# Optimization experiments

Hardware: AMD Instinct MI355X
Metric: run time of the kernel (lower is better)

## Reference

```python
import jax, jax.numpy as jnp
import numpy as np

# Constants mirroring FFTGADBase(feature_extractor='none', Npre=2000, block_size=64, overlap=16)
L = 0.24            # diffusion step size l
K_COEF = 0.03       # K = exp(logk), logk = log(0.03) fixed in RGB mode
EPS = 1e-8
BLOCK_SIZE = 64
OVERLAP = 16
NPRE = 2000
FFT_STEPS = 10
VAR_THRESH = 0.1
UNIF_FRAC = 0.7
B, H, W = 2, 1024, 1024
SH, SW = 128, 128


def _g(x, K):
    # Perona-Malik edge-stopping function (repo's g)
    return 1.0 / (1.0 + (x * x) / (K * K))


def _c(feats, K):
    # diffusion coefficients from channel-mean absolute finite differences
    cv = _g(jnp.mean(jnp.abs(feats[:, :, 1:, :] - feats[:, :, :-1, :]), axis=1, keepdims=True), K)
    ch = _g(jnp.mean(jnp.abs(feats[:, :, :, 1:] - feats[:, :, :, :-1]), axis=1, keepdims=True), K)
    return cv, ch  # cv: [B,1,H-1,W], ch: [B,1,H,W-1]


def _diffuse_step(cv, ch, I, l=L):
    # anisotropic diffusion stencil update (transmissions between neighbors)
    dv = I[:, :, 1:, :] - I[:, :, :-1, :]
    dh = I[:, :, :, 1:] - I[:, :, :, :-1]
    tv = l * cv * dv
    th = l * ch * dh
    I = I - jnp.pad(tv, ((0, 0), (0, 0), (1, 0), (0, 0))) + jnp.pad(tv, ((0, 0), (0, 0), (0, 1), (0, 0)))
    I = I - jnp.pad(th, ((0, 0), (0, 0), (0, 0), (1, 0))) + jnp.pad(th, ((0, 0), (0, 0), (0, 0), (0, 1)))
    return I


def _adjust_step(img, source, mask_inv):
    b, c, h, w = img.shape
    sh, sw = source.shape[2], source.shape[3]
    fy, fx = h // sh, w // sw
    # AdaptiveAvgPool2d((sh,sw)) with exact divisor == uniform 8x8 mean pool
    img_ss = img.reshape(b, c, sh, fy, sw, fx).mean(axis=(3, 5))
    ratio_ss = source / (img_ss + EPS)
    ratio_ss = jnp.where(mask_inv, 1.0, ratio_ss)
    # F.interpolate(mode='nearest') with exact multiple == pixel repeat
    ratio = jnp.repeat(jnp.repeat(ratio_ss, fy, axis=2), fx, axis=3)
    return img * ratio


def _avgpool3(x):
    # F.avg_pool2d(x, 3, stride=1, padding=1), count_include_pad=True -> /9 everywhere
    s = jax.lax.reduce_window(x, 0.0, jax.lax.add, (1, 1, 3, 3), (1, 1, 1, 1),
                              [(0, 0), (0, 0), (1, 1), (1, 1)])
    return s / 9.0


def _uniform_regions(cv, ch):
    cv_var = _avgpool3(cv ** 2) - _avgpool3(cv) ** 2
    ch_var = _avgpool3(ch ** 2) - _avgpool3(ch) ** 2
    hm = min(cv_var.shape[2], ch_var.shape[2])
    wm = min(cv_var.shape[3], ch_var.shape[3])
    return (cv_var[:, :, :hm, :wm] < VAR_THRESH) & (ch_var[:, :, :hm, :wm] < VAR_THRESH)


def _fft_block(block, cv_b, ch_b):
    # Closed-form multi-step uniform-coefficient diffusion in the Fourier domain:
    # eigenvalue of one explicit diffusion step on periodic grid, raised to FFT_STEPS.
    cv_m = cv_b.mean(axis=(1, 2, 3), keepdims=True)  # [B,1,1,1]
    ch_m = ch_b.mean(axis=(1, 2, 3), keepdims=True)
    bh, bw = block.shape[-2], block.shape[-1]
    fy = jnp.arange(bh, dtype=jnp.float32)[:, None]
    fx = jnp.arange(bw // 2 + 1, dtype=jnp.float32)[None, :]
    lam = (1.0 - 2.0 * L * cv_m * (1.0 - jnp.cos(2.0 * jnp.pi * fy / bh))
               - 2.0 * L * ch_m * (1.0 - jnp.cos(2.0 * jnp.pi * fx / bw)))
    Fb = jnp.fft.rfft2(block)
    return jnp.fft.irfft2(Fb * (lam ** FFT_STEPS), s=(bh, bw)).astype(block.dtype)


def _fft_diffuse(depth, cv, ch, ur):
    b, c, h, w = depth.shape
    h_cv, w_cv = cv.shape[2], cv.shape[3]
    h_ch, w_ch = ch.shape[2], ch.shape[3]
    step = BLOCK_SIZE - OVERLAP
    for y in range(0, h, step):
        for x in range(0, w, step):
            ye, xe = min(y + BLOCK_SIZE, h), min(x + BLOCK_SIZE, w)
            cye, cxe = min(ye - 1, h_cv), min(xe, w_cv)
            hye, hxe = min(ye, h_ch), min(xe - 1, w_ch)
            if y >= cye or x >= cxe or y >= hye or x >= hxe:
                continue
            uye, uxe = min(ye, ur.shape[2]), min(xe, ur.shape[3])
            if y >= uye or x >= uxe:
                continue
            old = depth[:, :, y:ye, x:xe]
            new = _fft_block(old, cv[:, :, y:cye, x:cxe], ch[:, :, y:hye, x:hxe])
            unif = ur[:, :, y:uye, x:uxe].astype(jnp.float32).mean(axis=(1, 2, 3))
            apply_fft = (unif > UNIF_FRAC)[:, None, None, None]
            bh, bw = ye - y, xe - x
            by = jnp.ones((bh,), dtype=jnp.float32)
            if y > 0:
                n = min(OVERLAP, bh)
                by = by.at[:n].set(jnp.arange(n, dtype=jnp.float32) / OVERLAP)
            bx = jnp.ones((bw,), dtype=jnp.float32)
            if x > 0:
                n = min(OVERLAP, bw)
                bx = bx.at[:n].set(jnp.arange(n, dtype=jnp.float32) / OVERLAP)
            blend = by[:, None] * bx[None, :]
            merged = old * (1.0 - blend) + new * blend  # at (0,0) blend==1 -> direct write, as in torch
            merged = jnp.where(apply_fft, merged, old)
            depth = depth.at[:, :, y:ye, x:xe].set(merged)
    return depth


def _diffuse(img, guide, source, mask_inv):
    # RGB mode: guide_feats = cat([guide, img], 1); K = exp(logk) = 0.03
    feats = jnp.concatenate([guide, img], axis=1)
    cv, ch = _c(feats, K_COEF)
    ur = _uniform_regions(cv, ch)
    # Npre section runs under torch.no_grad()
    img0 = jax.lax.stop_gradient(img)
    cv0 = jax.lax.stop_gradient(cv)
    ch0 = jax.lax.stop_gradient(ch)
    img0 = _fft_diffuse(img0, cv0, ch0, ur)

    def body(I, _):
        I = _diffuse_step(cv0, ch0, I)
        I = _adjust_step(I, jax.lax.stop_gradient(source), mask_inv)
        return I, None

    y_pred, _ = jax.lax.scan(body, img0, None, length=min(500, NPRE))
    return y_pred, cv, ch


def setup_inputs() -> dict:
    key = jax.random.key(0)
    k1, k2, k3, k4 = jax.random.split(key, 4)
    guide = jax.random.normal(k1, (B, 3, H, W), dtype=jnp.float32)
    # keep depths safely > deps=0.1 so the shift branch is statically off
    source = jax.random.uniform(k2, (B, 1, SH, SW), dtype=jnp.float32) + 0.5
    mask_lr = jax.random.uniform(k3, (B, 1, SH, SW), dtype=jnp.float32)
    y_bicubic = jnp.repeat(jnp.repeat(source, H // SH, axis=2), W // SW, axis=3) \
                + 0.05 * jax.random.normal(k4, (B, 1, H, W), dtype=jnp.float32)
    return {"guide": guide, "source": source, "mask_lr": mask_lr, "y_bicubic": y_bicubic}


def reference(guide, source, mask_lr, y_bicubic):
    mask_inv = mask_lr < 0.5
    y_pred, cv, ch = _diffuse(y_bicubic, guide, source, mask_inv)
    return y_pred, cv, ch
```

## Files before the change

### kernel.cpp

```cpp
#include <hip/hip_runtime.h>

#define HH 1024
#define WW 1024
#define HW 1048576
#define NBLK 22

__device__ __forceinline__ float aload(const float* p)
{
    return __uint_as_float(__hip_atomic_load((const unsigned int*)p,
                           __ATOMIC_RELAXED, __HIP_MEMORY_SCOPE_AGENT));
}
__device__ __forceinline__ void astore(float* p, float v)
{
    __hip_atomic_store((unsigned int*)p, __float_as_uint(v),
                       __ATOMIC_RELAXED, __HIP_MEMORY_SCOPE_AGENT);
}

__global__ __launch_bounds__(256) void coeff_kernel(
    const float* __restrict__ guide, const float* __restrict__ img,
    float* __restrict__ cv, float* __restrict__ ch)
{
    int x = blockIdx.x * 256 + threadIdx.x;
    int y = blockIdx.y;
    int b = blockIdx.z;
    const float* g0 = guide + (size_t)b * 3 * HW;
    const float* im = img + (size_t)b * HW;
    int p = y * WW + x;
    float f0 = g0[p], f1 = g0[HW + p], f2 = g0[2 * HW + p], f3 = im[p];
    const float KK = 0.03f * 0.03f;
    if (y < HH - 1) {
        int q = p + WW;
        float s = fabsf(g0[q] - f0) + fabsf(g0[HW + q] - f1)
                + fabsf(g0[2 * HW + q] - f2) + fabsf(im[q] - f3);
        float t = s * 0.25f;
        cv[(size_t)b * 1023 * 1024 + p] = 1.0f / (1.0f + t * t / KK);
    }
    if (x < WW - 1) {
        int q = p + 1;
        float s = fabsf(g0[q] - f0) + fabsf(g0[HW + q] - f1)
                + fabsf(g0[2 * HW + q] - f2) + fabsf(im[q] - f3);
        float t = s * 0.25f;
        ch[(size_t)b * 1024 * 1023 + y * 1023 + x] = 1.0f / (1.0f + t * t / KK);
    }
}

__device__ __forceinline__ float block_reduce(float v, float* tmp)
{
    #pragma unroll
    for (int off = 32; off > 0; off >>= 1) v += __shfl_down(v, off);
    __syncthreads();
    if ((threadIdx.x & 63) == 0) tmp[threadIdx.x >> 6] = v;
    __syncthreads();
    return tmp[0] + tmp[1] + tmp[2] + tmp[3];
}

__global__ __launch_bounds__(256) void stats_kernel(
    const float* __restrict__ cv, const float* __restrict__ ch,
    float* __restrict__ cvmA, float* __restrict__ chmA, float* __restrict__ unifA)
{
    int iy = blockIdx.x, ix = blockIdx.y, b = blockIdx.z;
    int y0 = iy * 48, x0 = ix * 48;
    int ye = min(y0 + 64, HH), xe = min(x0 + 64, WW);
    int bh = ye - y0, bw = xe - x0;
    const float* cvb = cv + (size_t)b * 1023 * 1024;
    const float* chb = ch + (size_t)b * 1024 * 1023;
    int tid = threadIdx.x;

    int cnt_cv = (bh - 1) * bw;
    float s_cv = 0.f;
    for (int k = tid; k < cnt_cv; k += 256) {
        int r = k / bw, c = k - r * bw;
        s_cv += cvb[(y0 + r) * 1024 + x0 + c];
    }
    int cnt_ch = bh * (bw - 1);
    float s_ch = 0.f;
    for (int k = tid; k < cnt_ch; k += 256) {
        int r = k / (bw - 1), c = k - r * (bw - 1);
        s_ch += chb[(y0 + r) * 1023 + x0 + c];
    }
    int uh = min(ye, 1023) - y0, uw = min(xe, 1023) - x0;
    int cnt_u = uh * uw;
    float s_u = 0.f;
    for (int k = tid; k < cnt_u; k += 256) {
        int r = k / uw, c = k - r * uw;
        int py = y0 + r, px = x0 + c;
        float a1 = 0.f, a2 = 0.f;
        #pragma unroll
        for (int dy = -1; dy <= 1; ++dy)
            #pragma unroll
            for (int dx = -1; dx <= 1; ++dx) {
                int yy = py + dy, xx = px + dx;
                if (yy >= 0 && yy < 1023 && xx >= 0 && xx < 1024) {
                    float v = cvb[yy * 1024 + xx]; a1 += v; a2 += v * v;
                }
            }
        float va = a2 * (1.f / 9.f) - (a1 * (1.f / 9.f)) * (a1 * (1.f / 9.f));
        float b1 = 0.f, b2 = 0.f;
        #pragma unroll
        for (int dy = -1; dy <= 1; ++dy)
            #pragma unroll
            for (int dx = -1; dx <= 1; ++dx) {
                int yy = py + dy, xx = px + dx;
                if (yy >= 0 && yy < 1024 && xx >= 0 && xx < 1023) {
                    float v = chb[yy * 1023 + xx]; b1 += v; b2 += v * v;
                }
            }
        float vb = b2 * (1.f / 9.f) - (b1 * (1.f / 9.f)) * (b1 * (1.f / 9.f));
        s_u += (va < 0.1f && vb < 0.1f) ? 1.f : 0.f;
    }

    __shared__ float tmp[4];
    float t_cv = block_reduce(s_cv, tmp);
    float t_ch = block_reduce(s_ch, tmp);
    float t_u  = block_reduce(s_u, tmp);
    if (tid == 0) {
        int bi = (b * NBLK + iy) * NBLK + ix;
        cvmA[bi]  = t_cv / (float)cnt_cv;
        chmA[bi]  = t_ch / (float)cnt_ch;
        unifA[bi] = t_u / (float)cnt_u;
    }
}

__global__ __launch_bounds__(256) void fftblk_group(
    float* __restrict__ depth,
    const float* __restrict__ cvmA, const float* __restrict__ chmA,
    const float* __restrict__ unifA, unsigned int* __restrict__ ftags,
    int base)
{
    int rem = base + (int)blockIdx.x;
    int iy = 0, ix = 0;
    for (int d = 0; d < 64; ++d) {
        int lo = (d > 21) ? ((d - 20) >> 1) : 0;
        int hi = ((d >> 1) < 21) ? (d >> 1) : 21;
        int wd = hi - lo + 1;
        if (rem < wd) { iy = lo + rem; ix = d - 2 * iy; break; }
        rem -= wd;
    }
    int b = blockIdx.y;
    int bi = (b * NBLK + iy) * NBLK + ix;
    int tid = threadIdx.x;

    bool active = (unifA[bi] > 0.7f);
    int y0 = iy * 48, x0 = ix * 48;
    int bh = min(64, HH - y0), bw = min(64, WW - x0);
    const int RH = bh >> 4;
    const int RW = bw >> 4;
    const int ty = tid >> 4, tx = tid & 15;
    float* gbase = depth + (size_t)b * HW + y0 * WW + x0;

    float cur[4][4], orig[4][4];
    if (active) {
        #pragma unroll
        for (int r = 0; r < 4; ++r)
            #pragma unroll
            for (int c = 0; c < 4; ++c)
                if (r < RH && c < RW) {
                    int i = RH * ty + r, j = RW * tx + c;
                    if (i >= 16 && j >= 16) {
                        float v = aload(gbase + i * WW + j);
                        cur[r][c] = v; orig[r][c] = v;
                    }
                }
    }

    {
        bool act = false; int di = 0, dj = 0;
        if (tid == 0) { act = (ix > 0);            di = iy;     dj = ix - 1; }
        if (tid == 1) { act = (iy > 0 && ix > 0);  di = iy - 1; dj = ix - 1; }
        if (tid == 2) { act = (iy > 0);            di = iy - 1; dj = ix;     }
        if (tid == 3) { act = (iy > 0 && ix < 21); di = iy - 1; dj = ix + 1; }
        if (tid < 4 && act) {
            const unsigned int* tp = ftags + (((b * NBLK + di) * NBLK + dj) << 4);
            int guard = 0;
            while (__hip_atomic_load(tp, __ATOMIC_RELAXED,
                                     __HIP_MEMORY_SCOPE_AGENT) < 1u) {
                if (++guard > (1 << 22)) break;
            }
        }
    }
    __syncthreads();

    if (active) {
        float av = 0.24f * cvmA[bi];
        float ah = 0.24f * chmA[bi];

        #pragma unroll
        for (int r = 0; r < 4; ++r)
            #pragma unroll
            for (int c = 0; c < 4; ++c)
                if (r < RH && c < RW) {
                    int i = RH * ty + r, j = RW * tx + c;
                    if (i < 16 || j < 16) {
                        float v = aload(gbase + i * WW + j);
                        cur[r][c] = v; orig[r][c] = v;
                    }
                }

        __shared__ float rT[2][16][65];
        __shared__ float rB[2][16][65];
        __shared__ float cL[2][16][65];
        __shared__ float cR[2][16][65];

        for (int it = 0; it < 10; ++it) {
            const int p = it & 1;
            #pragma unroll
            for (int c = 0; c < 4; ++c)
                if (c < RW) {
                    rT[p][ty][RW * tx + c] = cur[0][c];
                    rB[p][ty][RW * tx + c] = (RH == 4) ? cur[3][c] : cur[0][c];
                }
            #pragma unroll
            for (int r = 0; r < 4; ++r)
                if (r < RH) {
                    cL[p][tx][RH * ty + r] = cur[r][0];
                    cR[p][tx][RH * ty + r] = (RW == 4) ? cur[r][3] : cur[r][0];
                }
            __syncthreads();

            float nxt[4][4];
            #pragma unroll
            for (int r = 0; r < 4; ++r)
                #pragma unroll
                for (int c = 0; c < 4; ++c)
                    if (r < RH && c < RW) {
                        float ce = cur[r][c];
                        float up = (r > 0) ? cur[r - 1][c]
                                           : rB[p][(ty - 1) & 15][RW * tx + c];
                        float dn = rT[p][(ty + 1) & 15][RW * tx + c];
                        if (r + 1 < 4) { if (r + 1 < RH) dn = cur[r + 1][c]; }
                        float lf = (c > 0) ? cur[r][c - 1]
                                           : cR[p][(tx - 1) & 15][RH * ty + r];
                        float rt = cL[p][(tx + 1) & 15][RH * ty + r];
                        if (c + 1 < 4) { if (c + 1 < RW) rt = cur[r][c + 1]; }
                        nxt[r][c] = ce + av * (up + dn - 2.f * ce)
                                       + ah * (lf + rt - 2.f * ce);
                    }
            #pragma unroll
            for (int r = 0; r < 4; ++r)
                #pragma unroll
                for (int c = 0; c < 4; ++c)
                    if (r < RH && c < RW) cur[r][c] = nxt[r][c];
        }

        const float inv16 = 1.f / 16.f;
        #pragma unroll
        for (int r = 0; r < 4; ++r)
            #pragma unroll
            for (int c = 0; c < 4; ++c)
                if (r < RH && c < RW) {
                    int i = RH * ty + r, j = RW * tx + c;
                    float wy = (y0 > 0 && i < 16) ? (float)i * inv16 : 1.f;
                    float wx = (x0 > 0 && j < 16) ? (float)j * inv16 : 1.f;
                    float w = wy * wx;
                    astore(gbase + i * WW + j,
                           orig[r][c] * (1.f - w) + cur[r][c] * w);
                }
        asm volatile("s_waitcnt vmcnt(0)" ::: "memory");
    }
    __syncthreads();
    if (tid == 0)
        __hip_atomic_store(ftags + (bi << 4), 1u, __ATOMIC_RELAXED,
                           __HIP_MEMORY_SCOPE_AGENT);
}

__global__ __launch_bounds__(256, 4) void iter_kernel(
    const float* __restrict__ Iin, float* __restrict__ Iout,
    const float* __restrict__ cv, const float* __restrict__ ch,
    const float* __restrict__ source, const float* __restrict__ mask)
{
    const int w = blockIdx.x;
    const int xcd = w & 7, j = w >> 3;
    const int grb = xcd * 32 + (j >> 2);
    const int b  = grb >> 7;
    const int r0 = (grb & 127) * 8;
    const int c0 = (j & 3) * 256;
    const int tid = threadIdx.x;
    __shared__ float sI[10][258];
    const float* Ib  = Iin + (size_t)b * HW;
    const float* cvb = cv + (size_t)b * 1023 * 1024;
    const float* chb = ch + (size_t)b * 1024 * 1023;

    for (int k = tid; k < 10 * 258; k += 256) {
        int r = k / 258, c = k - r * 258;
        int gy = r0 - 1 + r, gx = c0 - 1 + c;
        float v = 0.f;
        if (gy >= 0 && gy < HH && gx >= 0 && gx < WW) v = Ib[gy * WW + gx];
        sI[r][c] = v;
    }

    const int gx = c0 + tid;
    float cvv[9];
    #pragma unroll
    for (int k = 0; k < 9; ++k) {
        int gr = r0 - 1 + k;
        cvv[k] = (gr >= 0 && gr < 1023) ? cvb[gr * 1024 + gx] : 0.f;
    }
    float chl[8], chh[8];
    #pragma unroll
    for (int k = 0; k < 8; ++k) {
        int rr = r0 + k;
        chh[k] = (gx < 1023) ? chb[rr * 1023 + gx] : 0.f;
        chl[k] = (gx > 0)    ? chb[rr * 1023 + gx - 1] : 0.f;
    }
    __syncthreads();

    float o[8];
    #pragma unroll
    for (int r = 0; r < 8; ++r) {
        float c  = sI[r + 1][tid + 1];
        float up = sI[r][tid + 1], dn = sI[r + 2][tid + 1];
        float lf = sI[r + 1][tid], rt = sI[r + 1][tid + 2];
        o[r] = c + 0.24f * ( cvv[r + 1] * (dn - c) - cvv[r] * (c - up)
                           + chh[r] * (rt - c)     - chl[r] * (c - lf) );
    }

    float colsum = 0.f;
    #pragma unroll
    for (int r = 0; r < 8; ++r) colsum += o[r];
    colsum += __shfl_xor(colsum, 1);
    colsum += __shfl_xor(colsum, 2);
    colsum += __shfl_xor(colsum, 4);
    float mean = colsum * (1.0f / 64.0f);

    int sy = r0 >> 3;
    int sx = (c0 >> 3) + (tid >> 3);
    int sidx = b * 128 * 128 + sy * 128 + sx;
    float ratio = (mask[sidx] < 0.5f) ? 1.0f : source[sidx] / (mean + 1e-8f);

    float* Ob = Iout + (size_t)b * HW;
    #pragma unroll
    for (int r = 0; r < 8; ++r)
        Ob[(r0 + r) * WW + c0 + tid] = o[r] * ratio;
}

__global__ __launch_bounds__(256, 1) void iter500_strip(
    float* __restrict__ depth,
    const float* __restrict__ cv, const float* __restrict__ ch,
    const float* __restrict__ source, const float* __restrict__ mask,
    float* __restrict__ rowbuf,
    unsigned int* __restrict__ tags,
    int niter)
{
    const int s   = blockIdx.x;
    const int b   = s >> 7;
    const int rb  = s & 127;
    const int r0  = rb * 8;
    const int tid = threadIdx.x;
    const int w   = tid >> 6;
    const int l   = tid & 63;
    const int gx0 = (w << 8) + (l << 2);
    const int swz = (w << 8) + l;

    __shared__ float sE[2][3][2][8];

    float* gdep = depth + (size_t)b * HW;

    float o[8][4];
    #pragma unroll
    for (int r = 0; r < 8; ++r) {
        float4 v = *(const float4*)(gdep + (size_t)(r0 + r) * WW + gx0);
        o[r][0] = v.x; o[r][1] = v.y; o[r][2] = v.z; o[r][3] = v.w;
    }
    unsigned int* mytag = tags + ((s * 4 + w) << 4);
    {
        float* dT = rowbuf + ((size_t)s * 2 + 0) * 1024 + swz;
        float* dB = rowbuf + ((size_t)s * 2 + 1) * 1024 + swz;
        #pragma unroll
        for (int c = 0; c < 4; ++c) { astore(dT + (c << 6), o[0][c]);
                                      astore(dB + (c << 6), o[7][c]); }
        asm volatile("s_waitcnt vmcnt(0)" ::: "memory");
        if (l == 0)
            __hip_atomic_store(mytag, 1u, __ATOMIC_RELAXED, __HIP_MEMORY_SCOPE_AGENT);
    }

    const float* cvb = cv + (size_t)b * 1023 * 1024;
    const float* chb = ch + (size_t)b * 1024 * 1023;
    float cvv[9][4];
    #pragma unroll
    for (int k = 0; k < 9; ++k) {
        int gr = r0 - 1 + k;
        #pragma unroll
        for (int c = 0; c < 4; ++c)
            cvv[k][c] = (gr >= 0 && gr < 1023) ? cvb[(size_t)gr * 1024 + gx0 + c] : 0.f;
    }
    float chh[8][4], chl0[8];
    #pragma unroll
    for (int k = 0; k < 8; ++k) {
        int rr = r0 + k;
        #pragma unroll
        for (int c = 0; c < 4; ++c)
            chh[k][c] = (gx0 + c < 1023) ? chb[(size_t)rr * 1023 + gx0 + c] : 0.f;
        chl0[k] = (gx0 > 0) ? chb[(size_t)rr * 1023 + gx0 - 1] : 0.f;
    }
    int sidx = b * 128 * 128 + rb * 128 + (gx0 >> 3);
    float sval = source[sidx];
    bool  adj  = (mask[sidx] >= 0.5f);

    const unsigned int* tagT = tags + ((((rb > 0   ? s - 1 : s) * 4) + w) << 4);
    const unsigned int* tagB = tags + ((((rb < 127 ? s + 1 : s) * 4) + w) << 4);

    for (int it = 0; it < niter; ++it) {
        const int p = it & 1;
        const int q = p ^ 1;

        if (l == 63 && w < 3) {
            #pragma unroll
            for (int r = 0; r < 8; ++r) sE[p][w][0][r] = o[r][3];
        }
        if (l == 0 && w > 0) {
            #pragma unroll
            for (int r = 0; r < 8; ++r) sE[p][w - 1][1][r] = o[r][0];
        }
        __syncthreads();

        float lfS[8], rtS[8];
        int wl = (w > 0) ? w - 1 : 0;
        int wr = (w < 3) ? w : 0;
        #pragma unroll
        for (int r = 0; r < 8; ++r) {
            float a  = __shfl(o[r][3], l - 1);
            float bq = __shfl(o[r][0], l + 1);
            lfS[r] = (l == 0)  ? ((w > 0) ? sE[p][wl][0][r] : 0.f) : a;
            rtS[r] = (l == 63) ? ((w < 3) ? sE[p][wr][1][r] : 0.f) : bq;
        }

        float n[8][4];
        float cs = 0.f;
        #pragma unroll
        for (int r = 1; r < 7; ++r) {
            #pragma unroll
            for (int c = 0; c < 4; ++c) {
                float cen = o[r][c];
                float up = o[r - 1][c];
                float dn = o[r + 1][c];
                float lf = (c == 0) ? lfS[r] : o[r][c - 1];
                float rt = (c == 3) ? rtS[r] : o[r][c + 1];
                float cl = (c == 0) ? chl0[r] : chh[r][c - 1];
                float v = cen + 0.24f * ( cvv[r + 1][c] * (dn - cen)
                                        - cvv[r][c]     * (cen - up)
                                        + chh[r][c]     * (rt - cen)
                                        - cl            * (cen - lf) );
                n[r][c] = v; cs += v;
            }
        }

        {
            unsigned int target = (unsigned int)(it + 1);
            bool active = (l == 0) ? (rb > 0) : ((l == 1) ? (rb < 127) : false);
            if (active) {
                const unsigned int* pp = (l == 0) ? tagT : tagB;
                int guard = 0;
                while (__hip_atomic_load(pp, __ATOMIC_RELAXED,
                                         __HIP_MEMORY_SCOPE_AGENT) < target) {
                    if (++guard > (1 << 18)) break;
                    __builtin_amdgcn_s_sleep(1);
                }
            }
        }
        asm volatile("" ::: "memory");

        float ht[4] = {0.f, 0.f, 0.f, 0.f}, hb[4] = {0.f, 0.f, 0.f, 0.f};
        if (rb > 0) {
            const float* srcp = rowbuf + (((size_t)p * 256 + (s - 1)) * 2 + 1) * 1024 + swz;
            #pragma unroll
            for (int c = 0; c < 4; ++c) ht[c] = aload(srcp + (c << 6));
        }
        if (rb < 127) {
            const float* srcp = rowbuf + (((size_t)p * 256 + (s + 1)) * 2 + 0) * 1024 + swz;
            #pragma unroll
            for (int c = 0; c < 4; ++c) hb[c] = aload(srcp + (c << 6));
        }

        #pragma unroll
        for (int c = 0; c < 4; ++c) {
            float cen = o[0][c];
            float up = ht[c], dn = o[1][c];
            float lf = (c == 0) ? lfS[0] : o[0][c - 1];
            float rt = (c == 3) ? rtS[0] : o[0][c + 1];
            float cl = (c == 0) ? chl0[0] : chh[0][c - 1];
            float v = cen + 0.24f * ( cvv[1][c] * (dn - cen) - cvv[0][c] * (cen - up)
                                    + chh[0][c] * (rt - cen) - cl * (cen - lf) );
            n[0][c] = v; cs += v;
        }
        #pragma unroll
        for (int c = 0; c < 4; ++c) {
            float cen = o[7][c];
            float up = o[6][c], dn = hb[c];
            float lf = (c == 0) ? lfS[7] : o[7][c - 1];
            float rt = (c == 3) ? rtS[7] : o[7][c + 1];
            float cl = (c == 0) ? chl0[7] : chh[7][c - 1];
            float v = cen + 0.24f * ( cvv[8][c] * (dn - cen) - cvv[7][c] * (cen - up)
                                    + chh[7][c] * (rt - cen) - cl * (cen - lf) );
            n[7][c] = v; cs += v;
        }

        cs += __shfl_xor(cs, 1);
        float mean  = cs * (1.0f / 64.0f);
        float ratio = adj ? sval / (mean + 1e-8f) : 1.0f;
        #pragma unroll
        for (int r = 0; r < 8; ++r)
            #pragma unroll
            for (int c = 0; c < 4; ++c) o[r][c] = n[r][c] * ratio;

        {
            float* dT = rowbuf + (((size_t)q * 256 + s) * 2 + 0) * 1024 + swz;
            float* dB = rowbuf + (((size_t)q * 256 + s) * 2 + 1) * 1024 + swz;
            #pragma unroll
            for (int c = 0; c < 4; ++c) { astore(dT + (c << 6), o[0][c]);
                                          astore(dB + (c << 6), o[7][c]); }
        }
        asm volatile("s_waitcnt vmcnt(0)" ::: "memory");
        if (l == 0)
            __hip_atomic_store(mytag, (unsigned int)(it + 2),
                               __ATOMIC_RELAXED, __HIP_MEMORY_SCOPE_AGENT);
    }

    #pragma unroll
    for (int r = 0; r < 8; ++r) {
        float4 v;
        v.x = o[r][0]; v.y = o[r][1]; v.z = o[r][2]; v.w = o[r][3];
        *(float4*)(gdep + (size_t)(r0 + r) * WW + gx0) = v;
    }
}

extern "C" void kernel_launch(void* const* d_in, const int* in_sizes, int n_in,
                              void* d_out, int out_size, void* d_ws, size_t ws_size,
                              hipStream_t stream)
{
    (void)in_sizes; (void)n_in; (void)out_size; (void)ws_size;
    const float* guide  = (const float*)d_in[0];
    const float* source = (const float*)d_in[1];
    const float* mask   = (const float*)d_in[2];
    const float* ybic   = (const float*)d_in[3];

    float* out   = (float*)d_out;
    float* ypred = out;
    float* cv    = out + 2097152;
    float* ch    = out + 2097152 + 2095104;

    float* wsf    = (float*)d_ws;
    float* dbuf   = wsf;
    float* rowbuf = wsf;
    unsigned int* itags = (unsigned int*)(wsf + 1048576);
    unsigned int* ftags = itags + 16384;
    float* cvmA   = wsf + 2097152;
    float* chmA   = cvmA + 2 * NBLK * NBLK;
    float* unifA  = chmA + 2 * NBLK * NBLK;

    static int persist_ok = -1;
    if (persist_ok < 0) {
        int dev = 0;
        (void)hipGetDevice(&dev);
        hipDeviceProp_t prop;
        int nCU = 0;
        if (hipGetDeviceProperties(&prop, dev) == hipSuccess)
            nCU = prop.multiProcessorCount;
        int nb = 0;
        hipError_t e = hipOccupancyMaxActiveBlocksPerMultiprocessor(
            &nb, iter500_strip, 256, 0);
        persist_ok = (e == hipSuccess && nCU > 0 && nb * nCU >= 256) ? 1 : 0;
    }

    coeff_kernel<<<dim3(4, HH, 2), 256, 0, stream>>>(guide, ybic, cv, ch);
    stats_kernel<<<dim3(NBLK, NBLK, 2), 256, 0, stream>>>(cv, ch, cvmA, chmA, unifA);
    hipMemcpyAsync(ypred, ybic, (size_t)2 * HW * sizeof(float),
                   hipMemcpyDeviceToDevice, stream);
    hipMemsetAsync(itags, 0, 2 * 16384 * sizeof(unsigned int), stream);

    fftblk_group<<<dim3(484, 2), 256, 0, stream>>>(
        ypred, cvmA, chmA, unifA, ftags, 0);

    if (persist_ok) {
        iter500_strip<<<dim3(256), 256, 0, stream>>>(
            ypred, cv, ch, source, mask, rowbuf, itags, 500);
    } else {
        for (int i = 0; i < 500; ++i) {
            const float* src = (i & 1) ? dbuf : ypred;
            float*       dst = (i & 1) ? ypred : dbuf;
            iter_kernel<<<dim3(1024), 256, 0, stream>>>(
                src, dst, cv, ch, source, mask);
        }
    }
}
```

Before: 2.146 ms.

## Process FFT-diffuse blocks as row wavefronts with left-overlap carried in shared memory

Replaces the 484x2 per-block grid, which relies on wavefront tag polling, with one workgroup per block-row that walks its 22 blocks left to right. The right 16-column overlap of each processed block is kept in shared memory for the next block, so the left-neighbor dependency no longer needs a global round trip or a tag wait. Each block now waits only on the two blocks above it, and the spin loop sleeps between polls. The cost is far less parallelism, only 44 workgroups run sequential chains, and inactive blocks still pass through the sync and shared-memory handoff.

```diff
diff --git a/kernel.cpp b/kernel.cpp
--- a/kernel.cpp
+++ b/kernel.cpp
@@ -121,146 +121,152 @@
     }
 }
 
-__global__ __launch_bounds__(256) void fftblk_group(
+__global__ __launch_bounds__(256) void fftrow_kernel(
     float* __restrict__ depth,
     const float* __restrict__ cvmA, const float* __restrict__ chmA,
-    const float* __restrict__ unifA, unsigned int* __restrict__ ftags,
-    int base)
-{
-    int rem = base + (int)blockIdx.x;
-    int iy = 0, ix = 0;
-    for (int d = 0; d < 64; ++d) {
-        int lo = (d > 21) ? ((d - 20) >> 1) : 0;
-        int hi = ((d >> 1) < 21) ? (d >> 1) : 21;
-        int wd = hi - lo + 1;
-        if (rem < wd) { iy = lo + rem; ix = d - 2 * iy; break; }
-        rem -= wd;
-    }
-    int b = blockIdx.y;
-    int bi = (b * NBLK + iy) * NBLK + ix;
-    int tid = threadIdx.x;
-
-    bool active = (unifA[bi] > 0.7f);
-    int y0 = iy * 48, x0 = ix * 48;
-    int bh = min(64, HH - y0), bw = min(64, WW - x0);
-    const int RH = bh >> 4;
-    const int RW = bw >> 4;
-    const int ty = tid >> 4, tx = tid & 15;
-    float* gbase = depth + (size_t)b * HW + y0 * WW + x0;
-
-    float cur[4][4], orig[4][4];
-    if (active) {
+    const float* __restrict__ unifA, unsigned int* __restrict__ ftags)
+{
+    const int iy  = blockIdx.x;
+    const int b   = blockIdx.y;
+    const int tid = threadIdx.x;
+    const int ty  = tid >> 4, tx = tid & 15;
+    const int y0  = iy * 48;
+    const int bh  = min(64, HH - y0);
+    const int RH  = bh >> 4;
+    float* gdep = depth + (size_t)b * HW;
+
+    __shared__ float rT[2][16][65];
+    __shared__ float rB[2][16][65];
+    __shared__ float cL[2][16][65];
+    __shared__ float cR[2][16][65];
+    __shared__ float prev[64][17];
+
+    for (int ix = 0; ix < NBLK; ++ix) {
+        const int x0 = ix * 48;
+        const int bw = min(64, WW - x0);
+        const int RW = bw >> 4;
+        const int bi = (b * NBLK + iy) * NBLK + ix;
+        float* gbase = gdep + (size_t)y0 * WW + x0;
+
+        float cur[4][4], orig[4][4];
+
         #pragma unroll
         for (int r = 0; r < 4; ++r)
             #pragma unroll
             for (int c = 0; c < 4; ++c)
                 if (r < RH && c < RW) {
                     int i = RH * ty + r, j = RW * tx + c;
-                    if (i >= 16 && j >= 16) {
+                    bool fromPrev = (ix > 0 && j < 16);
+                    if (!fromPrev && (i >= 16 || iy == 0)) {
+                        float v = gbase[i * WW + j];
+                        cur[r][c] = v; orig[r][c] = v;
+                    }
+                }
+
+        if (iy > 0) {
+            if (tid == 0 || (tid == 1 && ix < NBLK - 1)) {
+                int dj = (tid == 0) ? ix : ix + 1;
+                const unsigned int* tp =
+                    ftags + (((b * NBLK + (iy - 1)) * NBLK + dj) << 4);
+                int guard = 0;
+                while (__hip_atomic_load(tp, __ATOMIC_RELAXED,
+                                         __HIP_MEMORY_SCOPE_AGENT) < 1u) {
+                    if (++guard > (1 << 20)) break;
+                    __builtin_amdgcn_s_sleep(2);
+                }
+            }
+        }
+        __syncthreads();
+
+        #pragma unroll
+        for (int r = 0; r < 4; ++r)
+            #pragma unroll
+            for (int c = 0; c < 4; ++c)
+                if (r < RH && c < RW) {
+                    int i = RH * ty + r, j = RW * tx + c;
+                    bool fromPrev = (ix > 0 && j < 16);
+                    if (fromPrev) {
+                        float v = prev[i][j];
+                        cur[r][c] = v; orig[r][c] = v;
+                    } else if (i < 16 && iy > 0) {
                         float v = aload(gbase + i * WW + j);
                         cur[r][c] = v; orig[r][c] = v;
                     }
                 }
-    }
-
-    {
-        bool act = false; int di = 0, dj = 0;
-        if (tid == 0) { act = (ix > 0);            di = iy;     dj = ix - 1; }
-        if (tid == 1) { act = (iy > 0 && ix > 0);  di = iy - 1; dj = ix - 1; }
-        if (tid == 2) { act = (iy > 0);            di = iy - 1; dj = ix;     }
-        if (tid == 3) { act = (iy > 0 && ix < 21); di = iy - 1; dj = ix + 1; }
-        if (tid < 4 && act) {
-            const unsigned int* tp = ftags + (((b * NBLK + di) * NBLK + dj) << 4);
-            int guard = 0;
-            while (__hip_atomic_load(tp, __ATOMIC_RELAXED,
-                                     __HIP_MEMORY_SCOPE_AGENT) < 1u) {
-                if (++guard > (1 << 22)) break;
+
+        bool active = (unifA[bi] > 0.7f);
+        if (active) {
+            float av = 0.24f * cvmA[bi];
+            float ah = 0.24f * chmA[bi];
+            for (int it = 0; it < 10; ++it) {
+                const int p = it & 1;
+                #pragma unroll
+                for (int c = 0; c < 4; ++c)
+                    if (c < RW) {
+                        rT[p][ty][RW * tx + c] = cur[0][c];
+                        rB[p][ty][RW * tx + c] = (RH == 4) ? cur[3][c] : cur[0][c];
+                    }
+                #pragma unroll
+                for (int r = 0; r < 4; ++r)
+                    if (r < RH) {
+                        cL[p][tx][RH * ty + r] = cur[r][0];
+                        cR[p][tx][RH * ty + r] = (RW == 4) ? cur[r][3] : cur[r][0];
+                    }
+                __syncthreads();
+
+                float nxt[4][4];
+                #pragma unroll
+                for (int r = 0; r < 4; ++r)
+                    #pragma unroll
+                    for (int c = 0; c < 4; ++c)
+                        if (r < RH && c < RW) {
+                            float ce = cur[r][c];
+                            float up = (r > 0) ? cur[r - 1][c]
+                                               : rB[p][(ty - 1) & 15][RW * tx + c];
+                            float dn = rT[p][(ty + 1) & 15][RW * tx + c];
+                            if (r + 1 < 4) { if (r + 1 < RH) dn = cur[r + 1][c]; }
+                            float lf = (c > 0) ? cur[r][c - 1]
+                                               : cR[p][(tx - 1) & 15][RH * ty + r];
+                            float rt = cL[p][(tx + 1) & 15][RH * ty + r];
+                            if (c + 1 < 4) { if (c + 1 < RW) rt = cur[r][c + 1]; }
+                            nxt[r][c] = ce + av * (up + dn - 2.f * ce)
+                                           + ah * (lf + rt - 2.f * ce);
+                        }
+                #pragma unroll
+                for (int r = 0; r < 4; ++r)
+                    #pragma unroll
+                    for (int c = 0; c < 4; ++c)
+                        if (r < RH && c < RW) cur[r][c] = nxt[r][c];
             }
         }
-    }
-    __syncthreads();
-
-    if (active) {
-        float av = 0.24f * cvmA[bi];
-        float ah = 0.24f * chmA[bi];
-
+
+        __syncthreads();
+        const float inv16 = 1.f / 16.f;
         #pragma unroll
         for (int r = 0; r < 4; ++r)
             #pragma unroll
             for (int c = 0; c < 4; ++c)
                 if (r < RH && c < RW) {
                     int i = RH * ty + r, j = RW * tx + c;
-                    if (i < 16 || j < 16) {
-                        float v = aload(gbase + i * WW + j);
-                        cur[r][c] = v; orig[r][c] = v;
+                    float wv;
+                    if (active) {
+                        float wy = (y0 > 0 && i < 16) ? (float)i * inv16 : 1.f;
+                        float wx = (x0 > 0 && j < 16) ? (float)j * inv16 : 1.f;
+                        float w = wy * wx;
+                        wv = orig[r][c] * (1.f - w) + cur[r][c] * w;
+                        astore(gbase + i * WW + j, wv);
+                    } else {
+                        wv = orig[r][c];
                     }
-                }
-
-        __shared__ float rT[2][16][65];
-        __shared__ float rB[2][16][65];
-        __shared__ float cL[2][16][65];
-        __shared__ float cR[2][16][65];
-
-        for (int it = 0; it < 10; ++it) {
-            const int p = it & 1;
-            #pragma unroll
-            for (int c = 0; c < 4; ++c)
-                if (c < RW) {
-                    rT[p][ty][RW * tx + c] = cur[0][c];
-                    rB[p][ty][RW * tx + c] = (RH == 4) ? cur[3][c] : cur[0][c];
-                }
-            #pragma unroll
-            for (int r = 0; r < 4; ++r)
-                if (r < RH) {
-                    cL[p][tx][RH * ty + r] = cur[r][0];
-                    cR[p][tx][RH * ty + r] = (RW == 4) ? cur[r][3] : cur[r][0];
-                }
-            __syncthreads();
-
-            float nxt[4][4];
-            #pragma unroll
-            for (int r = 0; r < 4; ++r)
-                #pragma unroll
-                for (int c = 0; c < 4; ++c)
-                    if (r < RH && c < RW) {
-                        float ce = cur[r][c];
-                        float up = (r > 0) ? cur[r - 1][c]
-                                           : rB[p][(ty - 1) & 15][RW * tx + c];
-                        float dn = rT[p][(ty + 1) & 15][RW * tx + c];
-                        if (r + 1 < 4) { if (r + 1 < RH) dn = cur[r + 1][c]; }
-                        float lf = (c > 0) ? cur[r][c - 1]
-                                           : cR[p][(tx - 1) & 15][RH * ty + r];
-                        float rt = cL[p][(tx + 1) & 15][RH * ty + r];
-                        if (c + 1 < 4) { if (c + 1 < RW) rt = cur[r][c + 1]; }
-                        nxt[r][c] = ce + av * (up + dn - 2.f * ce)
-                                       + ah * (lf + rt - 2.f * ce);
-                    }
-            #pragma unroll
-            for (int r = 0; r < 4; ++r)
-                #pragma unroll
-                for (int c = 0; c < 4; ++c)
-                    if (r < RH && c < RW) cur[r][c] = nxt[r][c];
-        }
-
-        const float inv16 = 1.f / 16.f;
-        #pragma unroll
-        for (int r = 0; r < 4; ++r)
-            #pragma unroll
-            for (int c = 0; c < 4; ++c)
-                if (r < RH && c < RW) {
-                    int i = RH * ty + r, j = RW * tx + c;
-                    float wy = (y0 > 0 && i < 16) ? (float)i * inv16 : 1.f;
-                    float wx = (x0 > 0 && j < 16) ? (float)j * inv16 : 1.f;
-                    float w = wy * wx;
-                    astore(gbase + i * WW + j,
-                           orig[r][c] * (1.f - w) + cur[r][c] * w);
-                }
-        asm volatile("s_waitcnt vmcnt(0)" ::: "memory");
-    }
-    __syncthreads();
-    if (tid == 0)
-        __hip_atomic_store(ftags + (bi << 4), 1u, __ATOMIC_RELAXED,
-                           __HIP_MEMORY_SCOPE_AGENT);
+                    if (j >= 48) prev[i][j - 48] = wv;
+                }
+        if (active)
+            asm volatile("s_waitcnt vmcnt(0)" ::: "memory");
+        __syncthreads();
+        if (tid == 0)
+            __hip_atomic_store(ftags + (bi << 4), 1u, __ATOMIC_RELAXED,
+                               __HIP_MEMORY_SCOPE_AGENT);
+    }
 }
 
 __global__ __launch_bounds__(256, 4) void iter_kernel(
@@ -567,8 +573,8 @@
                    hipMemcpyDeviceToDevice, stream);
     hipMemsetAsync(itags, 0, 2 * 16384 * sizeof(unsigned int), stream);
 
-    fftblk_group<<<dim3(484, 2), 256, 0, stream>>>(
-        ypred, cvmA, chmA, unifA, ftags, 0);
+    fftrow_kernel<<<dim3(NBLK, 2), 256, 0, stream>>>(
+        ypred, cvmA, chmA, unifA, ftags);
 
     if (persist_ok) {
         iter500_strip<<<dim3(256), 256, 0, stream>>>(
```

Measured after the change: 2.276 ms. +6.1%, slower.

## Run per-block FFT diffusion as single wavefront using DPP permutes instead of LDS

Applied to the files above, without the earlier changes.

Rewrites the overlapped-block diffusion kernel so each block is handled by one 64-lane wavefront, with each lane owning a full column in registers. Horizontal neighbours come from ds_bpermute and vertical neighbours from the lane's own registers, which removes shared-memory staging and the per-iteration __syncthreads. Spin waits on neighbour tags now sleep between polls, and the guard limit is lowered. The cost is higher register use (128 floats per lane) and fewer threads per block, which may serialize more work along the dependency wavefront.

```diff
diff --git a/kernel.cpp b/kernel.cpp
--- a/kernel.cpp
+++ b/kernel.cpp
@@ -121,13 +121,12 @@
     }
 }
 
-__global__ __launch_bounds__(256) void fftblk_group(
+__global__ __launch_bounds__(64) void fftwave_kernel(
     float* __restrict__ depth,
     const float* __restrict__ cvmA, const float* __restrict__ chmA,
-    const float* __restrict__ unifA, unsigned int* __restrict__ ftags,
-    int base)
-{
-    int rem = base + (int)blockIdx.x;
+    const float* __restrict__ unifA, unsigned int* __restrict__ ftags)
+{
+    int rem = (int)blockIdx.x;
     int iy = 0, ix = 0;
     for (int d = 0; d < 64; ++d) {
         int lo = (d > 21) ? ((d - 20) >> 1) : 0;
@@ -136,129 +135,98 @@
         if (rem < wd) { iy = lo + rem; ix = d - 2 * iy; break; }
         rem -= wd;
     }
-    int b = blockIdx.y;
-    int bi = (b * NBLK + iy) * NBLK + ix;
-    int tid = threadIdx.x;
-
-    bool active = (unifA[bi] > 0.7f);
-    int y0 = iy * 48, x0 = ix * 48;
-    int bh = min(64, HH - y0), bw = min(64, WW - x0);
-    const int RH = bh >> 4;
-    const int RW = bw >> 4;
-    const int ty = tid >> 4, tx = tid & 15;
-    float* gbase = depth + (size_t)b * HW + y0 * WW + x0;
-
-    float cur[4][4], orig[4][4];
-    if (active) {
-        #pragma unroll
-        for (int r = 0; r < 4; ++r)
-            #pragma unroll
-            for (int c = 0; c < 4; ++c)
-                if (r < RH && c < RW) {
-                    int i = RH * ty + r, j = RW * tx + c;
-                    if (i >= 16 && j >= 16) {
-                        float v = aload(gbase + i * WW + j);
-                        cur[r][c] = v; orig[r][c] = v;
-                    }
-                }
+    const int b  = blockIdx.y;
+    const int bi = (b * NBLK + iy) * NBLK + ix;
+    const int l  = threadIdx.x;
+
+    const bool active = (unifA[bi] > 0.7f);
+    const int y0 = iy * 48, x0 = ix * 48;
+    const int bh = min(64, HH - y0), bw = min(64, WW - x0);
+    float* gbase = depth + (size_t)b * HW + (size_t)y0 * WW + x0;
+
+    float cur[64], orig[64];
+
+    if (active && l < bw) {
+        #pragma unroll
+        for (int i = 0; i < 64; ++i) {
+            bool wr = (iy > 0 && i < 16) || (ix > 0 && l < 16);
+            if (i < bh && !wr) {
+                float v = gbase[i * WW + l];
+                cur[i] = v; orig[i] = v;
+            }
+        }
     }
 
     {
         bool act = false; int di = 0, dj = 0;
-        if (tid == 0) { act = (ix > 0);            di = iy;     dj = ix - 1; }
-        if (tid == 1) { act = (iy > 0 && ix > 0);  di = iy - 1; dj = ix - 1; }
-        if (tid == 2) { act = (iy > 0);            di = iy - 1; dj = ix;     }
-        if (tid == 3) { act = (iy > 0 && ix < 21); di = iy - 1; dj = ix + 1; }
-        if (tid < 4 && act) {
+        if (l == 0) { act = (ix > 0);            di = iy;     dj = ix - 1; }
+        if (l == 1) { act = (iy > 0 && ix > 0);  di = iy - 1; dj = ix - 1; }
+        if (l == 2) { act = (iy > 0);            di = iy - 1; dj = ix;     }
+        if (l == 3) { act = (iy > 0 && ix < 21); di = iy - 1; dj = ix + 1; }
+        if (l < 4 && act) {
             const unsigned int* tp = ftags + (((b * NBLK + di) * NBLK + dj) << 4);
             int guard = 0;
             while (__hip_atomic_load(tp, __ATOMIC_RELAXED,
                                      __HIP_MEMORY_SCOPE_AGENT) < 1u) {
-                if (++guard > (1 << 22)) break;
-            }
-        }
-    }
-    __syncthreads();
+                if (++guard > (1 << 20)) break;
+                __builtin_amdgcn_s_sleep(2);
+            }
+        }
+    }
+    asm volatile("" ::: "memory");
 
     if (active) {
-        float av = 0.24f * cvmA[bi];
-        float ah = 0.24f * chmA[bi];
-
-        #pragma unroll
-        for (int r = 0; r < 4; ++r)
-            #pragma unroll
-            for (int c = 0; c < 4; ++c)
-                if (r < RH && c < RW) {
-                    int i = RH * ty + r, j = RW * tx + c;
-                    if (i < 16 || j < 16) {
-                        float v = aload(gbase + i * WW + j);
-                        cur[r][c] = v; orig[r][c] = v;
+        if (l < bw) {
+            #pragma unroll
+            for (int i = 0; i < 64; ++i) {
+                bool wr = (iy > 0 && i < 16) || (ix > 0 && l < 16);
+                if (i < bh && wr) {
+                    float v = aload(gbase + i * WW + l);
+                    cur[i] = v; orig[i] = v;
+                }
+            }
+        }
+
+        if (l < bw) {
+            const int mask = bw - 1;
+            const int la = (((l - 1) & mask)) << 2;
+            const int ra = (((l + 1) & mask)) << 2;
+            const float av = 0.24f * cvmA[bi];
+            const float ah = 0.24f * chmA[bi];
+            for (int it = 0; it < 10; ++it) {
+                float first_old = cur[0];
+                float above = (bh == 64) ? cur[63] : cur[15];
+                #pragma unroll
+                for (int i = 0; i < 64; ++i) {
+                    if (i < bh) {
+                        float oldv = cur[i];
+                        float dn = first_old;
+                        if (i + 1 < 64) { if (i + 1 < bh) dn = cur[i + 1]; }
+                        float lf = __uint_as_float(__builtin_amdgcn_ds_bpermute(
+                                       la, __float_as_uint(oldv)));
+                        float rt = __uint_as_float(__builtin_amdgcn_ds_bpermute(
+                                       ra, __float_as_uint(oldv)));
+                        cur[i] = oldv + av * (above + dn - 2.f * oldv)
+                                      + ah * (lf + rt - 2.f * oldv);
+                        above = oldv;
                     }
                 }
-
-        __shared__ float rT[2][16][65];
-        __shared__ float rB[2][16][65];
-        __shared__ float cL[2][16][65];
-        __shared__ float cR[2][16][65];
-
-        for (int it = 0; it < 10; ++it) {
-            const int p = it & 1;
-            #pragma unroll
-            for (int c = 0; c < 4; ++c)
-                if (c < RW) {
-                    rT[p][ty][RW * tx + c] = cur[0][c];
-                    rB[p][ty][RW * tx + c] = (RH == 4) ? cur[3][c] : cur[0][c];
+            }
+
+            const float inv16 = 1.f / 16.f;
+            float wx = (x0 > 0 && l < 16) ? (float)l * inv16 : 1.f;
+            #pragma unroll
+            for (int i = 0; i < 64; ++i)
+                if (i < bh) {
+                    float wy = (y0 > 0 && i < 16) ? (float)i * inv16 : 1.f;
+                    float w = wy * wx;
+                    astore(gbase + i * WW + l,
+                           orig[i] + w * (cur[i] - orig[i]));
                 }
-            #pragma unroll
-            for (int r = 0; r < 4; ++r)
-                if (r < RH) {
-                    cL[p][tx][RH * ty + r] = cur[r][0];
-                    cR[p][tx][RH * ty + r] = (RW == 4) ? cur[r][3] : cur[r][0];
-                }
-            __syncthreads();
-
-            float nxt[4][4];
-            #pragma unroll
-            for (int r = 0; r < 4; ++r)
-                #pragma unroll
-                for (int c = 0; c < 4; ++c)
-                    if (r < RH && c < RW) {
-                        float ce = cur[r][c];
-                        float up = (r > 0) ? cur[r - 1][c]
-                                           : rB[p][(ty - 1) & 15][RW * tx + c];
-                        float dn = rT[p][(ty + 1) & 15][RW * tx + c];
-                        if (r + 1 < 4) { if (r + 1 < RH) dn = cur[r + 1][c]; }
-                        float lf = (c > 0) ? cur[r][c - 1]
-                                           : cR[p][(tx - 1) & 15][RH * ty + r];
-                        float rt = cL[p][(tx + 1) & 15][RH * ty + r];
-                        if (c + 1 < 4) { if (c + 1 < RW) rt = cur[r][c + 1]; }
-                        nxt[r][c] = ce + av * (up + dn - 2.f * ce)
-                                       + ah * (lf + rt - 2.f * ce);
-                    }
-            #pragma unroll
-            for (int r = 0; r < 4; ++r)
-                #pragma unroll
-                for (int c = 0; c < 4; ++c)
-                    if (r < RH && c < RW) cur[r][c] = nxt[r][c];
-        }
-
-        const float inv16 = 1.f / 16.f;
-        #pragma unroll
-        for (int r = 0; r < 4; ++r)
-            #pragma unroll
-            for (int c = 0; c < 4; ++c)
-                if (r < RH && c < RW) {
-                    int i = RH * ty + r, j = RW * tx + c;
-                    float wy = (y0 > 0 && i < 16) ? (float)i * inv16 : 1.f;
-                    float wx = (x0 > 0 && j < 16) ? (float)j * inv16 : 1.f;
-                    float w = wy * wx;
-                    astore(gbase + i * WW + j,
-                           orig[r][c] * (1.f - w) + cur[r][c] * w);
-                }
+        }
         asm volatile("s_waitcnt vmcnt(0)" ::: "memory");
     }
-    __syncthreads();
-    if (tid == 0)
+    if (l == 0)
         __hip_atomic_store(ftags + (bi << 4), 1u, __ATOMIC_RELAXED,
                            __HIP_MEMORY_SCOPE_AGENT);
 }
@@ -567,8 +535,8 @@
                    hipMemcpyDeviceToDevice, stream);
     hipMemsetAsync(itags, 0, 2 * 16384 * sizeof(unsigned int), stream);
 
-    fftblk_group<<<dim3(484, 2), 256, 0, stream>>>(
-        ypred, cvmA, chmA, unifA, ftags, 0);
+    fftwave_kernel<<<dim3(484, 2), 64, 0, stream>>>(
+        ypred, cvmA, chmA, unifA, ftags);
 
     if (persist_ok) {
         iter500_strip<<<dim3(256), 256, 0, stream>>>(
```

After: 3.550 ms. 1.65x slower.
